# Kernel tuning notes

Hardware: AMD Instinct MI355X
Metric: run time of the kernel (lower is better)

## Reference

```python
import jax, jax.numpy as jnp
import numpy as np
from jax import lax

B, N, D = 4, 4096, 2048
E = 128            # expand_ratio = head dim
H = D // E         # 16 heads
CHUNK = 64
EPS = 1e-6


def setup_inputs() -> dict:
    key = jax.random.key(0)
    ks = jax.random.split(key, 6)
    std = 0.02
    x = jax.random.normal(ks[0], (B, N, D), dtype=jnp.float32)
    Wq = jax.random.normal(ks[1], (D, D), dtype=jnp.float32) * std
    Wk = jax.random.normal(ks[2], (D, D), dtype=jnp.float32) * std
    Wv = jax.random.normal(ks[3], (D, D), dtype=jnp.float32) * std
    Wo = jax.random.normal(ks[4], (D, D), dtype=jnp.float32) * std
    norm_w = jnp.ones((D,), dtype=jnp.float32)
    return {"x": x, "Wq": Wq, "Wk": Wk, "Wv": Wv, "Wo": Wo, "norm_w": norm_w}


def rmsnorm(x, w):
    var = jnp.mean(jnp.square(x), axis=-1, keepdims=True)
    return x * lax.rsqrt(var + EPS) * w


def chunked_gla(q, v, log_f):
    """Gated linear attention with per-channel ('vector') decay.

    Recurrence (per batch b, head h):
        S_t = diag(f_t) S_{t-1} + outer(k_t, v_t),  k_t = 1 - f_t = 1 - exp(log_f_t)
        o_t = q_t @ S_t
    Computed with an IO-aware chunked scan (intra-chunk matmul + inter-chunk state).
    q, v, log_f: [B, N, H, E] -> returns o: [B, N, H, E]
    """
    b, n, h, e = q.shape
    nc = n // CHUNK
    k = 1.0 - jnp.exp(log_f)

    def to_chunks(t):  # [B,N,H,E] -> [NC,B,C,H,E]
        return t.reshape(b, nc, CHUNK, h, e).transpose(1, 0, 2, 3, 4)

    qs, ks_, vs, lfs = map(to_chunks, (q, k, v, log_f))
    A = jnp.cumsum(lfs, axis=2)  # inclusive cumulative log-decay within chunk
    mask = jnp.tril(jnp.ones((CHUNK, CHUNK), dtype=bool))  # causal within chunk

    def step(S, xs):
        qc, kc, vc, Ac = xs            # [B,C,H,E]; S: [B,H,E,E]
        q_dec = qc * jnp.exp(Ac)       # q_t * prod_{r<=t} f_r
        k_dec = kc * jnp.exp(-Ac)
        # intra-chunk: scores[t,s] = <q_t * exp(A_t - A_s), k_s>, causal
        scores = jnp.einsum('bthe,bshe->bhts', q_dec, k_dec)
        scores = jnp.where(mask[None, None], scores, 0.0)
        o_intra = jnp.einsum('bhts,bshe->bthe', scores, vc)
        # inter-chunk: decayed query against carried state
        o_inter = jnp.einsum('bthe,bhef->bthf', q_dec, S)
        # state update to end of chunk
        A_last = Ac[:, -1]                              # [B,H,E]
        k_rem = kc * jnp.exp(A_last[:, None] - Ac)      # decay from s to chunk end
        S_new = jnp.exp(A_last)[..., None] * S + jnp.einsum('bthe,bthf->bhef', k_rem, vc)
        return S_new, o_intra + o_inter

    S0 = jnp.zeros((b, h, e, e), dtype=q.dtype)
    _, o = lax.scan(step, S0, (qs, ks_, vs, A))
    return o.transpose(1, 0, 2, 3, 4).reshape(b, n, h, e)


def reference(x, Wq, Wk, Wv, Wo, norm_w):
    b, n, d = x.shape
    q = jax.nn.silu(x @ Wq.T)                 # q_act = silu
    f = jax.nn.sigmoid(x @ Wk.T)              # f = sigmoid(k_proj(x))
    log_f = jax.nn.log_sigmoid(f)             # as in source (lower_bound is None)
    v = x @ Wv.T
    q, v, log_f = (t.reshape(b, n, H, E) for t in (q, v, log_f))
    o = chunked_gla(q, v, log_f)              # [B,N,H,E]
    o = o.reshape(b, n, d)
    o = rmsnorm(o, norm_w)
    return o @ Wo.T
```

## Files before the change

### kernel.cpp

```cpp
#include <hip/hip_runtime.h>
#include <cstdint>
#include <cstddef>

#define EPI_NONE 0
#define EPI_SILU 1
#define EPI_LOGSIG 2

typedef __attribute__((ext_vector_type(8))) short bf16x8;
typedef __attribute__((ext_vector_type(4))) float f32x4;

__device__ __forceinline__ float us2f(unsigned short u) {
    unsigned int x = ((unsigned int)u) << 16;
    return __uint_as_float(x);
}
__device__ __forceinline__ unsigned short f2us(float f) {
    unsigned int x = __float_as_uint(f);
    unsigned int r = (x + 0x7fffu + ((x >> 16) & 1u)) >> 16;
    return (unsigned short)r;
}

__device__ __forceinline__ void gl_lds16(const unsigned short* g, unsigned short* l) {
    __builtin_amdgcn_global_load_lds(
        (const __attribute__((address_space(1))) void*)g,
        (__attribute__((address_space(3))) void*)l, 16, 0, 0);
}

__global__ __launch_bounds__(256) void cast_bf16(const float* __restrict__ in,
                                                 unsigned short* __restrict__ out, int n8)
{
    int i = blockIdx.x * blockDim.x + threadIdx.x;
    if (i >= n8) return;
    const float4* p = (const float4*)(in + (size_t)i * 8);
    float4 a = p[0], b = p[1];
    __align__(16) unsigned short u[8];
    u[0] = f2us(a.x); u[1] = f2us(a.y); u[2] = f2us(a.z); u[3] = f2us(a.w);
    u[4] = f2us(b.x); u[5] = f2us(b.y); u[6] = f2us(b.z); u[7] = f2us(b.w);
    *(uint4*)(out + (size_t)i * 8) = *(const uint4*)u;
}

template<int EPI, bool OUT_BF16>
__global__ __launch_bounds__(256) void gemm_bt_mfma(const unsigned short* __restrict__ A,
                                                    const unsigned short* __restrict__ B,
                                                    void* __restrict__ Cv,
                                                    int M, int N, int K)
{
    __shared__ unsigned short As[128 * 32];
    __shared__ unsigned short Bs[128 * 32];

    const int tid  = threadIdx.x;
    const int lane = tid & 63;
    const int wv   = tid >> 6;
    const int m0   = blockIdx.y * 128;
    const int n0   = blockIdx.x * 128;
    const int wr   = (wv >> 1) * 64;
    const int wc   = (wv & 1) * 64;

    const int srow = wv * 16 + (lane >> 2);
    const int scol = (lane & 3) * 8;
    const unsigned short* Ag0 = A + (size_t)(m0 + srow) * K + scol;
    const unsigned short* Ag1 = Ag0 + (size_t)64 * K;
    const unsigned short* Bg0 = B + (size_t)(n0 + srow) * K + scol;
    const unsigned short* Bg1 = Bg0 + (size_t)64 * K;
    unsigned short* Al0 = As + wv * 512;
    unsigned short* Al1 = As + (4 + wv) * 512;
    unsigned short* Bl0 = Bs + wv * 512;
    unsigned short* Bl1 = Bs + (4 + wv) * 512;

    f32x4 acc[4][4];
#pragma unroll
    for (int i = 0; i < 4; ++i)
#pragma unroll
        for (int j = 0; j < 4; ++j) acc[i][j] = (f32x4){0.f, 0.f, 0.f, 0.f};

    const int fr = lane & 15;
    const int fk = (lane >> 4) * 8;

    for (int k0 = 0; k0 < K; k0 += 32) {
        __syncthreads();
        gl_lds16(Ag0 + k0, Al0);
        gl_lds16(Ag1 + k0, Al1);
        gl_lds16(Bg0 + k0, Bl0);
        gl_lds16(Bg1 + k0, Bl1);
        __syncthreads();

        bf16x8 af[4], bfr[4];
#pragma unroll
        for (int ti = 0; ti < 4; ++ti)
            af[ti] = *(const bf16x8*)&As[(wr + ti * 16 + fr) * 32 + fk];
#pragma unroll
        for (int tj = 0; tj < 4; ++tj)
            bfr[tj] = *(const bf16x8*)&Bs[(wc + tj * 16 + fr) * 32 + fk];
#pragma unroll
        for (int ti = 0; ti < 4; ++ti)
#pragma unroll
            for (int tj = 0; tj < 4; ++tj)
                acc[ti][tj] = __builtin_amdgcn_mfma_f32_16x16x32_bf16(
                    af[ti], bfr[tj], acc[ti][tj], 0, 0, 0);
    }

    const int crow = (lane >> 4) * 4;
    const int ccol = lane & 15;
#pragma unroll
    for (int ti = 0; ti < 4; ++ti) {
#pragma unroll
        for (int r = 0; r < 4; ++r) {
            const int row = m0 + wr + ti * 16 + crow + r;
#pragma unroll
            for (int tj = 0; tj < 4; ++tj) {
                float z = acc[ti][tj][r];
                if (EPI == EPI_SILU) {
                    z = z / (1.f + __expf(-z));
                } else if (EPI == EPI_LOGSIG) {
                    float s = 1.f / (1.f + __expf(-z));
                    z = -log1pf(__expf(-s));
                }
                const int col = n0 + wc + tj * 16 + ccol;
                if (OUT_BF16)
                    ((unsigned short*)Cv)[(size_t)row * N + col] = f2us(z);
                else
                    ((float*)Cv)[(size_t)row * N + col] = z;
            }
        }
    }
}

__global__ __launch_bounds__(256) void gla_a1(unsigned short* __restrict__ qb,
                                              unsigned short* __restrict__ lfb,
                                              const unsigned short* __restrict__ vb,
                                              unsigned short* __restrict__ obf,
                                              float* __restrict__ dbuf)
{
    __shared__ unsigned short q_sh[64][136];
    __shared__ unsigned short kd_sh[64][136];
    __shared__ unsigned short vT[128][72];
    __shared__ unsigned short sc[64][72];

    const int tid = threadIdx.x;
    const int bid = blockIdx.x;
    const int c = bid >> 6, bh = bid & 63;
    const int b = bh >> 4, h = bh & 15;
    const size_t tok0 = ((size_t)b * 4096 + (size_t)c * 64) * 2048 + (size_t)h * 128;

#pragma unroll
    for (int k = 0; k < 4; ++k) {
        int vi = tid + k * 256;
        int t = vi >> 4, e8 = (vi & 15) << 3;
        *(uint4*)&q_sh[t][e8]  = *(const uint4*)(qb  + tok0 + (size_t)t * 2048 + e8);
        *(uint4*)&kd_sh[t][e8] = *(const uint4*)(lfb + tok0 + (size_t)t * 2048 + e8);
    }
    if (tid < 128) {
        int t8 = tid >> 4, f8 = tid & 15;
        __align__(16) unsigned short a[8][8];
#pragma unroll
        for (int r = 0; r < 8; ++r)
            *(uint4*)a[r] = *(const uint4*)(vb + tok0 + (size_t)(t8 * 8 + r) * 2048 + f8 * 8);
#pragma unroll
        for (int j = 0; j < 8; ++j) {
            __align__(16) unsigned short w8[8];
#pragma unroll
            for (int r = 0; r < 8; ++r) w8[r] = a[r][j];
            *(uint4*)&vT[f8 * 8 + j][t8 * 8] = *(const uint4*)w8;
        }
    }
    __syncthreads();
    if (tid < 128) {
        const int e = tid;
        float a = 0.f;
        for (int t = 0; t < 64; ++t) {
            float lf = us2f(kd_sh[t][e]);
            a += lf;
            q_sh[t][e]  = f2us(us2f(q_sh[t][e]) * __expf(a));
            kd_sh[t][e] = f2us((1.f - __expf(lf)) * __expf(-a));
        }
        dbuf[(size_t)bid * 128 + e] = __expf(a);
    }
    __syncthreads();
#pragma unroll
    for (int k = 0; k < 4; ++k) {
        int vi = tid + k * 256;
        int t = vi >> 4, e8 = (vi & 15) << 3;
        *(uint4*)(qb  + tok0 + (size_t)t * 2048 + e8) = *(const uint4*)&q_sh[t][e8];
        *(uint4*)(lfb + tok0 + (size_t)t * 2048 + e8) = *(const uint4*)&kd_sh[t][e8];
    }

    const int lane = tid & 63, w = tid >> 6;
    const int fr = lane & 15, fq = lane >> 4;

    f32x4 sacc[4];
#pragma unroll
    for (int j = 0; j < 4; ++j) sacc[j] = (f32x4){0.f, 0.f, 0.f, 0.f};
#pragma unroll
    for (int ke = 0; ke < 4; ++ke) {
        bf16x8 af = *(const bf16x8*)&q_sh[16 * w + fr][ke * 32 + fq * 8];
#pragma unroll
        for (int tj = 0; tj < 4; ++tj) {
            bf16x8 bfv = *(const bf16x8*)&kd_sh[16 * tj + fr][ke * 32 + fq * 8];
            sacc[tj] = __builtin_amdgcn_mfma_f32_16x16x32_bf16(af, bfv, sacc[tj], 0, 0, 0);
        }
    }
#pragma unroll
    for (int tj = 0; tj < 4; ++tj)
#pragma unroll
        for (int r = 0; r < 4; ++r) {
            int trow = 16 * w + fq * 4 + r;
            int scol = 16 * tj + fr;
            sc[trow][scol] = f2us(scol <= trow ? sacc[tj][r] : 0.f);
        }
    __syncthreads();
    f32x4 oacc[8];
#pragma unroll
    for (int j = 0; j < 8; ++j) oacc[j] = (f32x4){0.f, 0.f, 0.f, 0.f};
#pragma unroll
    for (int ks = 0; ks < 2; ++ks) {
        bf16x8 af = *(const bf16x8*)&sc[16 * w + fr][ks * 32 + fq * 8];
#pragma unroll
        for (int tf = 0; tf < 8; ++tf) {
            bf16x8 bfv = *(const bf16x8*)&vT[16 * tf + fr][ks * 32 + fq * 8];
            oacc[tf] = __builtin_amdgcn_mfma_f32_16x16x32_bf16(af, bfv, oacc[tf], 0, 0, 0);
        }
    }
#pragma unroll
    for (int tf = 0; tf < 8; ++tf) {
        __align__(8) unsigned short o4[4];
#pragma unroll
        for (int r = 0; r < 4; ++r) o4[r] = f2us(oacc[tf][r]);
        *(uint2*)(obf + (((size_t)bid * 4 + w) * 8 + tf) * 256 + lane * 4) = *(const uint2*)o4;
    }
}

__global__ __launch_bounds__(256) void gla_a2(const unsigned short* __restrict__ lfb,
                                              const unsigned short* __restrict__ vb,
                                              const float* __restrict__ dbuf,
                                              unsigned short* __restrict__ UT)
{
    __shared__ unsigned short vT[128][72];
    __shared__ unsigned short kdT[128][72];
    __shared__ float d_sh[128];

    const int tid = threadIdx.x;
    const int bid = blockIdx.x;
    const int c = bid >> 6, bh = bid & 63;
    const int b = bh >> 4, h = bh & 15;
    const size_t tok0 = ((size_t)b * 4096 + (size_t)c * 64) * 2048 + (size_t)h * 128;

    if (tid < 128) {
        int t8 = tid >> 4, f8 = tid & 15;
        __align__(16) unsigned short a[8][8];
#pragma unroll
        for (int r = 0; r < 8; ++r)
            *(uint4*)a[r] = *(const uint4*)(vb + tok0 + (size_t)(t8 * 8 + r) * 2048 + f8 * 8);
#pragma unroll
        for (int j = 0; j < 8; ++j) {
            __align__(16) unsigned short w8[8];
#pragma unroll
            for (int r = 0; r < 8; ++r) w8[r] = a[r][j];
            *(uint4*)&vT[f8 * 8 + j][t8 * 8] = *(const uint4*)w8;
        }
        d_sh[tid] = dbuf[(size_t)bid * 128 + tid];
    } else {
        int i = tid - 128;
        int t8 = i >> 4, e8b = i & 15;
        __align__(16) unsigned short a[8][8];
#pragma unroll
        for (int r = 0; r < 8; ++r)
            *(uint4*)a[r] = *(const uint4*)(lfb + tok0 + (size_t)(t8 * 8 + r) * 2048 + e8b * 8);
#pragma unroll
        for (int j = 0; j < 8; ++j) {
            __align__(16) unsigned short w8[8];
#pragma unroll
            for (int r = 0; r < 8; ++r) w8[r] = a[r][j];
            *(uint4*)&kdT[e8b * 8 + j][t8 * 8] = *(const uint4*)w8;
        }
    }
    __syncthreads();

    const int lane = tid & 63, w = tid >> 6;
    const int fr = lane & 15, fq = lane >> 4;

    f32x4 acc[2][8];
#pragma unroll
    for (int mi = 0; mi < 2; ++mi)
#pragma unroll
        for (int te = 0; te < 8; ++te) acc[mi][te] = (f32x4){0.f, 0.f, 0.f, 0.f};
#pragma unroll
    for (int kt = 0; kt < 2; ++kt) {
        bf16x8 af0 = *(const bf16x8*)&vT[16 * (2 * w + 0) + fr][kt * 32 + fq * 8];
        bf16x8 af1 = *(const bf16x8*)&vT[16 * (2 * w + 1) + fr][kt * 32 + fq * 8];
#pragma unroll
        for (int te = 0; te < 8; ++te) {
            bf16x8 bfv = *(const bf16x8*)&kdT[16 * te + fr][kt * 32 + fq * 8];
            acc[0][te] = __builtin_amdgcn_mfma_f32_16x16x32_bf16(af0, bfv, acc[0][te], 0, 0, 0);
            acc[1][te] = __builtin_amdgcn_mfma_f32_16x16x32_bf16(af1, bfv, acc[1][te], 0, 0, 0);
        }
    }
    unsigned short* up = UT + (size_t)bid * 16384;
#pragma unroll
    for (int mi = 0; mi < 2; ++mi)
#pragma unroll
        for (int te = 0; te < 8; ++te) {
            int e = 16 * te + fr;
            float dv = d_sh[e];
#pragma unroll
            for (int r = 0; r < 4; ++r) {
                int f = 32 * w + 16 * mi + fq * 4 + r;
                up[f * 128 + e] = f2us(acc[mi][te][r] * dv);
            }
        }
}

__global__ __launch_bounds__(256) void gla_scan(unsigned short* __restrict__ UT,
                                                const float* __restrict__ dbuf)
{
    const int tid = threadIdx.x;
    const int bh = blockIdx.x >> 3, fs = blockIdx.x & 7;
    const int f = fs * 16 + (tid >> 4);
    const int e8 = (tid & 15) << 3;
    float S[8];
#pragma unroll
    for (int j = 0; j < 8; ++j) S[j] = 0.f;
    for (int c = 0; c < 64; ++c) {
        const size_t cb = (size_t)(c * 64 + bh);
        const size_t loc = cb * 16384 + (size_t)f * 128 + e8;
        uint4 uu = *(const uint4*)(UT + loc);
        float4 d0 = *(const float4*)(dbuf + cb * 128 + e8);
        float4 d1 = *(const float4*)(dbuf + cb * 128 + e8 + 4);
        __align__(16) unsigned short us8[8];
        *(uint4*)us8 = uu;
        __align__(16) unsigned short so[8];
#pragma unroll
        for (int j = 0; j < 8; ++j) so[j] = f2us(S[j]);
        *(uint4*)(UT + loc) = *(const uint4*)so;
        float dd[8] = {d0.x, d0.y, d0.z, d0.w, d1.x, d1.y, d1.z, d1.w};
#pragma unroll
        for (int j = 0; j < 8; ++j) S[j] = fmaf(dd[j], S[j], us2f(us8[j]));
    }
}

__global__ __launch_bounds__(256) void gla_c(unsigned short* __restrict__ qb,
                                             const unsigned short* __restrict__ UT,
                                             const unsigned short* __restrict__ obf)
{
    __shared__ unsigned short q_sh[64][136];
    __shared__ unsigned short ST_sh[128][136];

    const int tid = threadIdx.x;
    const int bid = blockIdx.x;
    const int c = bid >> 6, bh = bid & 63;
    const int b = bh >> 4, h = bh & 15;
    const size_t tok0 = ((size_t)b * 4096 + (size_t)c * 64) * 2048 + (size_t)h * 128;

#pragma unroll
    for (int k = 0; k < 4; ++k) {
        int vi = tid + k * 256;
        int t = vi >> 4, e8 = (vi & 15) << 3;
        *(uint4*)&q_sh[t][e8] = *(const uint4*)(qb + tok0 + (size_t)t * 2048 + e8);
    }
    const unsigned short* stp = UT + (size_t)bid * 16384;
#pragma unroll
    for (int k = 0; k < 8; ++k) {
        int vi = tid + k * 256;
        int f = vi >> 4, e8 = (vi & 15) << 3;
        *(uint4*)&ST_sh[f][e8] = *(const uint4*)(stp + (size_t)f * 128 + e8);
    }
    const int lane = tid & 63, w = tid >> 6;
    const int fr = lane & 15, fq = lane >> 4;

    f32x4 acc[8];
#pragma unroll
    for (int tf = 0; tf < 8; ++tf) {
        uint2 iv = *(const uint2*)(obf + (((size_t)bid * 4 + w) * 8 + tf) * 256 + lane * 4);
        __align__(8) unsigned short s4[4];
        *(uint2*)s4 = iv;
        acc[tf] = (f32x4){us2f(s4[0]), us2f(s4[1]), us2f(s4[2]), us2f(s4[3])};
    }
    __syncthreads();
#pragma unroll
    for (int ke = 0; ke < 4; ++ke) {
        bf16x8 af = *(const bf16x8*)&q_sh[16 * w + fr][ke * 32 + fq * 8];
#pragma unroll
        for (int tf = 0; tf < 8; ++tf) {
            bf16x8 bfv = *(const bf16x8*)&ST_sh[16 * tf + fr][ke * 32 + fq * 8];
            acc[tf] = __builtin_amdgcn_mfma_f32_16x16x32_bf16(af, bfv, acc[tf], 0, 0, 0);
        }
    }
#pragma unroll
    for (int tf = 0; tf < 8; ++tf)
#pragma unroll
        for (int r = 0; r < 4; ++r) {
            int t = 16 * w + fq * 4 + r;
            qb[tok0 + (size_t)t * 2048 + 16 * tf + fr] = f2us(acc[tf][r]);
        }
}

__global__ __launch_bounds__(256) void rmsnorm_kernel(unsigned short* __restrict__ o,
                                                      const float* __restrict__ w)
{
    __shared__ float red[4];
    const int row = blockIdx.x;
    const int tid = threadIdx.x;
    unsigned short* p = o + (size_t)row * 2048 + tid * 8;
    __align__(16) unsigned short u[8];
    *(uint4*)u = *(const uint4*)p;
    float f[8];
    float ss = 0.f;
#pragma unroll
    for (int j = 0; j < 8; ++j) { f[j] = us2f(u[j]); ss = fmaf(f[j], f[j], ss); }
#pragma unroll
    for (int off = 32; off > 0; off >>= 1) ss += __shfl_down(ss, off, 64);
    if ((tid & 63) == 0) red[tid >> 6] = ss;
    __syncthreads();
    float tot = red[0] + red[1] + red[2] + red[3];
    float scale = rsqrtf(tot * (1.f / 2048.f) + 1e-6f);
    const float* wp = w + tid * 8;
#pragma unroll
    for (int j = 0; j < 8; ++j) u[j] = f2us(f[j] * scale * wp[j]);
    *(uint4*)p = *(const uint4*)u;
}

extern "C" void kernel_launch(void* const* d_in, const int* in_sizes, int n_in,
                              void* d_out, int out_size, void* d_ws, size_t ws_size,
                              hipStream_t stream)
{
    const float* x  = (const float*)d_in[0];
    const float* Wq = (const float*)d_in[1];
    const float* Wk = (const float*)d_in[2];
    const float* Wv = (const float*)d_in[3];
    const float* Wo = (const float*)d_in[4];
    const float* nw = (const float*)d_in[5];
    float* out = (float*)d_out;

    const int M = 16384, N = 2048, K = 2048;
    const size_t S1 = (size_t)M * N;
    const size_t SW = (size_t)N * K;
    const size_t UTsz = (size_t)4096 * 16384;

    unsigned short* xb  = (unsigned short*)d_ws;
    unsigned short* Wqb = xb + S1;
    unsigned short* Wkb = Wqb + SW;
    unsigned short* Wvb = Wkb + SW;
    unsigned short* Wob = Wvb + SW;
    unsigned short* qb  = Wob + SW;
    unsigned short* vbf = qb + S1;
    unsigned short* lfb = vbf + S1;
    unsigned short* obf = lfb + S1;
    unsigned short* UT  = obf + S1;
    float* dbuf = (float*)(UT + UTsz);

    cast_bf16<<<(int)(S1 / 8 / 256), 256, 0, stream>>>(x, xb, (int)(S1 / 8));
    cast_bf16<<<(int)(SW / 8 / 256), 256, 0, stream>>>(Wq, Wqb, (int)(SW / 8));
    cast_bf16<<<(int)(SW / 8 / 256), 256, 0, stream>>>(Wk, Wkb, (int)(SW / 8));
    cast_bf16<<<(int)(SW / 8 / 256), 256, 0, stream>>>(Wv, Wvb, (int)(SW / 8));
    cast_bf16<<<(int)(SW / 8 / 256), 256, 0, stream>>>(Wo, Wob, (int)(SW / 8));

    dim3 gg(N / 128, M / 128);
    gemm_bt_mfma<EPI_SILU,  true><<<gg, 256, 0, stream>>>(xb, Wqb, qb,  M, N, K);
    gemm_bt_mfma<EPI_LOGSIG,true><<<gg, 256, 0, stream>>>(xb, Wkb, lfb, M, N, K);
    gemm_bt_mfma<EPI_NONE,  true><<<gg, 256, 0, stream>>>(xb, Wvb, vbf, M, N, K);

    gla_a1<<<4096, 256, 0, stream>>>(qb, lfb, vbf, obf, dbuf);
    gla_a2<<<4096, 256, 0, stream>>>(lfb, vbf, dbuf, UT);
    gla_scan<<<512, 256, 0, stream>>>(UT, dbuf);
    gla_c<<<4096, 256, 0, stream>>>(qb, UT, obf);

    rmsnorm_kernel<<<16384, 256, 0, stream>>>(qb, nw);
    gemm_bt_mfma<EPI_NONE, false><<<gg, 256, 0, stream>>>(qb, Wob, out, M, N, K);
}
```

Measured before the change: 1.356 ms.

## Double GEMM K-tile with XOR-swizzled LDS, staged bf16 epilogue, swapped grid order

```diff
diff --git a/kernel.cpp b/kernel.cpp
--- a/kernel.cpp
+++ b/kernel.cpp
@@ -44,27 +44,33 @@
                                                     void* __restrict__ Cv,
                                                     int M, int N, int K)
 {
-    __shared__ unsigned short As[128 * 32];
-    __shared__ unsigned short Bs[128 * 32];
+    __shared__ unsigned short smem[17408];
+    unsigned short* As = smem;
+    unsigned short* Bs = smem + 8192;
 
     const int tid  = threadIdx.x;
     const int lane = tid & 63;
     const int wv   = tid >> 6;
-    const int m0   = blockIdx.y * 128;
-    const int n0   = blockIdx.x * 128;
+    const int m0   = blockIdx.x * 128;
+    const int n0   = blockIdx.y * 128;
     const int wr   = (wv >> 1) * 64;
     const int wc   = (wv & 1) * 64;
 
-    const int srow = wv * 16 + (lane >> 2);
-    const int scol = (lane & 3) * 8;
-    const unsigned short* Ag0 = A + (size_t)(m0 + srow) * K + scol;
-    const unsigned short* Ag1 = Ag0 + (size_t)64 * K;
-    const unsigned short* Bg0 = B + (size_t)(n0 + srow) * K + scol;
-    const unsigned short* Bg1 = Bg0 + (size_t)64 * K;
-    unsigned short* Al0 = As + wv * 512;
-    unsigned short* Al1 = As + (4 + wv) * 512;
-    unsigned short* Bl0 = Bs + wv * 512;
-    unsigned short* Bl1 = Bs + (4 + wv) * 512;
+    const int lrow8 = lane >> 3;
+    const int xcol  = ((lane & 7) ^ lrow8) << 3;
+    const unsigned short* Ag[4];
+    const unsigned short* Bg[4];
+    unsigned short* Al[4];
+    unsigned short* Bl[4];
+#pragma unroll
+    for (int j = 0; j < 4; ++j) {
+        const int seg = j * 4 + wv;
+        const int row = seg * 8 + lrow8;
+        Ag[j] = A + (size_t)(m0 + row) * K + xcol;
+        Bg[j] = B + (size_t)(n0 + row) * K + xcol;
+        Al[j] = As + seg * 512;
+        Bl[j] = Bs + seg * 512;
+    }
 
     f32x4 acc[4][4];
 #pragma unroll
@@ -73,54 +79,84 @@
         for (int j = 0; j < 4; ++j) acc[i][j] = (f32x4){0.f, 0.f, 0.f, 0.f};
 
     const int fr = lane & 15;
-    const int fk = (lane >> 4) * 8;
-
-    for (int k0 = 0; k0 < K; k0 += 32) {
+    const int fq = lane >> 4;
+    const int rx = fr & 7;
+
+    for (int k0 = 0; k0 < K; k0 += 64) {
         __syncthreads();
-        gl_lds16(Ag0 + k0, Al0);
-        gl_lds16(Ag1 + k0, Al1);
-        gl_lds16(Bg0 + k0, Bl0);
-        gl_lds16(Bg1 + k0, Bl1);
+#pragma unroll
+        for (int j = 0; j < 4; ++j) {
+            gl_lds16(Ag[j] + k0, Al[j]);
+            gl_lds16(Bg[j] + k0, Bl[j]);
+        }
         __syncthreads();
 
-        bf16x8 af[4], bfr[4];
-#pragma unroll
-        for (int ti = 0; ti < 4; ++ti)
-            af[ti] = *(const bf16x8*)&As[(wr + ti * 16 + fr) * 32 + fk];
-#pragma unroll
-        for (int tj = 0; tj < 4; ++tj)
-            bfr[tj] = *(const bf16x8*)&Bs[(wc + tj * 16 + fr) * 32 + fk];
-#pragma unroll
-        for (int ti = 0; ti < 4; ++ti)
+#pragma unroll
+        for (int ks = 0; ks < 2; ++ks) {
+            const int ka = (((ks << 2) + fq) ^ rx) << 3;
+            bf16x8 af[4], bfv[4];
+#pragma unroll
+            for (int ti = 0; ti < 4; ++ti)
+                af[ti] = *(const bf16x8*)&As[(wr + ti * 16 + fr) * 64 + ka];
 #pragma unroll
             for (int tj = 0; tj < 4; ++tj)
-                acc[ti][tj] = __builtin_amdgcn_mfma_f32_16x16x32_bf16(
-                    af[ti], bfr[tj], acc[ti][tj], 0, 0, 0);
+                bfv[tj] = *(const bf16x8*)&Bs[(wc + tj * 16 + fr) * 64 + ka];
+#pragma unroll
+            for (int ti = 0; ti < 4; ++ti)
+#pragma unroll
+                for (int tj = 0; tj < 4; ++tj)
+                    acc[ti][tj] = __builtin_amdgcn_mfma_f32_16x16x32_bf16(
+                        af[ti], bfv[tj], acc[ti][tj], 0, 0, 0);
+        }
     }
 
     const int crow = (lane >> 4) * 4;
     const int ccol = lane & 15;
-#pragma unroll
-    for (int ti = 0; ti < 4; ++ti) {
-#pragma unroll
-        for (int r = 0; r < 4; ++r) {
-            const int row = m0 + wr + ti * 16 + crow + r;
-#pragma unroll
-            for (int tj = 0; tj < 4; ++tj) {
-                float z = acc[ti][tj][r];
-                if (EPI == EPI_SILU) {
-                    z = z / (1.f + __expf(-z));
-                } else if (EPI == EPI_LOGSIG) {
-                    float s = 1.f / (1.f + __expf(-z));
-                    z = -log1pf(__expf(-s));
+
+    if (OUT_BF16) {
+        __syncthreads();
+        unsigned short* Cs = smem;
+#pragma unroll
+        for (int ti = 0; ti < 4; ++ti)
+#pragma unroll
+            for (int r = 0; r < 4; ++r)
+#pragma unroll
+                for (int tj = 0; tj < 4; ++tj) {
+                    float z = acc[ti][tj][r];
+                    if (EPI == EPI_SILU) {
+                        z = z / (1.f + __expf(-z));
+                    } else if (EPI == EPI_LOGSIG) {
+                        float s = 1.f / (1.f + __expf(-z));
+                        z = -log1pf(__expf(-s));
+                    }
+                    Cs[(wr + ti * 16 + crow + r) * 136 + wc + tj * 16 + ccol] = f2us(z);
                 }
-                const int col = n0 + wc + tj * 16 + ccol;
-                if (OUT_BF16)
-                    ((unsigned short*)Cv)[(size_t)row * N + col] = f2us(z);
-                else
-                    ((float*)Cv)[(size_t)row * N + col] = z;
+        __syncthreads();
+        const int row = tid >> 1, half = tid & 1;
+        const unsigned short* src = &Cs[row * 136 + half * 64];
+        unsigned short* dst = (unsigned short*)Cv + (size_t)(m0 + row) * N + n0 + half * 64;
+#pragma unroll
+        for (int i = 0; i < 8; ++i)
+            *(uint4*)(dst + i * 8) = *(const uint4*)(src + i * 8);
+    } else {
+        float* C = (float*)Cv;
+#pragma unroll
+        for (int ti = 0; ti < 4; ++ti)
+#pragma unroll
+            for (int r = 0; r < 4; ++r) {
+                const int row = m0 + wr + ti * 16 + crow + r;
+#pragma unroll
+                for (int tj = 0; tj < 4; ++tj) {
+                    float z = acc[ti][tj][r];
+                    if (EPI == EPI_SILU) {
+                        z = z / (1.f + __expf(-z));
+                    } else if (EPI == EPI_LOGSIG) {
+                        float s = 1.f / (1.f + __expf(-z));
+                        z = -log1pf(__expf(-s));
+                    }
+                    C[(size_t)row * N + n0 + wc + tj * 16 + ccol] = z;
+                }
             }
-        }
     }
 }
 
@@ -452,7 +488,7 @@
     cast_bf16<<<(int)(SW / 8 / 256), 256, 0, stream>>>(Wv, Wvb, (int)(SW / 8));
     cast_bf16<<<(int)(SW / 8 / 256), 256, 0, stream>>>(Wo, Wob, (int)(SW / 8));
 
-    dim3 gg(N / 128, M / 128);
+    dim3 gg(M / 128, N / 128);
     gemm_bt_mfma<EPI_SILU,  true><<<gg, 256, 0, stream>>>(xb, Wqb, qb,  M, N, K);
     gemm_bt_mfma<EPI_LOGSIG,true><<<gg, 256, 0, stream>>>(xb, Wkb, lfb, M, N, K);
     gemm_bt_mfma<EPI_NONE,  true><<<gg, 256, 0, stream>>>(xb, Wvb, vbf, M, N, K);
```

After: 1.349 ms. About the same (-0.6%).
